# Performance work log

Hardware: AMD Instinct MI355X
Metric: run time of the kernel (lower is better)

The kernel has to match this reference:

```python
import jax, jax.numpy as jnp
import numpy as np


def _slice_coeffs(grid, guide):
    """Trilinear slice of bilateral grid at (x, y, guide) per full-res pixel.
    grid:  [B, C, D, Hg, Wg]  (C=12 affine coeffs)
    guide: [B, 1, H, W] in [0, 1]
    returns coeffs [B, C, H, W]
    """
    B, C, D, Hg, Wg = grid.shape
    H, W = guide.shape[2], guide.shape[3]
    g = guide[:, 0]  # [B, H, W]

    # HDRNet sampling convention: pixel centers mapped into grid coords
    gx = (jnp.arange(W, dtype=grid.dtype) + 0.5) / W * Wg - 0.5   # [W]
    gy = (jnp.arange(H, dtype=grid.dtype) + 0.5) / H * Hg - 0.5   # [H]
    gz = g * D - 0.5                                              # [B, H, W]

    gx = jnp.broadcast_to(gx[None, None, :], (B, H, W))
    gy = jnp.broadcast_to(gy[None, :, None], (B, H, W))

    fx0 = jnp.floor(gx); fy0 = jnp.floor(gy); fz0 = jnp.floor(gz)
    wx = gx - fx0; wy = gy - fy0; wz = gz - fz0  # trilinear fractions

    x0 = jnp.clip(fx0.astype(jnp.int32), 0, Wg - 1)
    x1 = jnp.clip(fx0.astype(jnp.int32) + 1, 0, Wg - 1)
    y0 = jnp.clip(fy0.astype(jnp.int32), 0, Hg - 1)
    y1 = jnp.clip(fy0.astype(jnp.int32) + 1, 0, Hg - 1)
    z0 = jnp.clip(fz0.astype(jnp.int32), 0, D - 1)
    z1 = jnp.clip(fz0.astype(jnp.int32) + 1, 0, D - 1)

    def gather_one(gb, zi, yi, xi):
        # gb: [C, D, Hg, Wg]; zi/yi/xi: [H, W] -> [C, H, W]
        return gb[:, zi, yi, xi]

    gather = jax.vmap(gather_one)  # over batch

    out = jnp.zeros((B, C, H, W), dtype=grid.dtype)
    for zi, wzc in ((z0, 1.0 - wz), (z1, wz)):
        for yi, wyc in ((y0, 1.0 - wy), (y1, wy)):
            for xi, wxc in ((x0, 1.0 - wx), (x1, wx)):
                w = (wzc * wyc * wxc)[:, None]  # [B, 1, H, W]
                out = out + w * gather(grid, zi, yi, xi)
    return out


def setup_inputs() -> dict:
    key = jax.random.key(0)
    k1, k2, k3 = jax.random.split(key, 3)
    Bilterial_Grid = jax.random.normal(k1, (4, 12, 8, 16, 16), dtype=jnp.float32)
    Guide = jax.random.uniform(k2, (4, 1, 1024, 1024), dtype=jnp.float32)
    fr = jax.random.uniform(k3, (4, 3, 1024, 1024), dtype=jnp.float32)
    return {"Bilterial_Grid": Bilterial_Grid, "Guide": Guide, "fr": fr}


def reference(Bilterial_Grid, Guide, fr):
    B, _, H, W = fr.shape
    coeffs = _slice_coeffs(Bilterial_Grid, Guide)          # [B, 12, H, W]
    co = coeffs.reshape(B, 3, 4, H, W)                      # 3x4 affine per pixel
    # out_c = sum_i A[c,i] * fr_i + b[c]
    out = jnp.einsum('boihw,bihw->bohw', co[:, :, :3], fr) + co[:, :, 3]
    return out
```

## Files before the change

### kernel.cpp

```cpp
#include <hip/hip_runtime.h>


#define ZSTRIDE 100

using half2v = decltype(__builtin_amdgcn_cvt_pkrtz(0.0f, 0.0f));

static __device__ __forceinline__ half2v pkrtz(float lo, float hi) {
    return __builtin_amdgcn_cvt_pkrtz(lo, hi);
}
static __device__ __forceinline__ half2v u2h2(unsigned int u) {
    return __builtin_bit_cast(half2v, u);
}
static __device__ __forceinline__ unsigned int h2u(half2v h) {
    return __builtin_bit_cast(unsigned int, h);
}

#if __has_builtin(__builtin_amdgcn_fdot2)
#define DOT2(d, wp, acc) __builtin_amdgcn_fdot2(u2h2(d), (wp), (acc), false)
#else
static __device__ __forceinline__ float dot2_sw(unsigned int d, half2v wp, float acc) {
    half2v h = u2h2(d);
    return fmaf((float)wp.x, (float)h.x, fmaf((float)wp.y, (float)h.y, acc));
}
#define DOT2(d, wp, acc) dot2_sw((d), (wp), (acc))
#endif

static __device__ __forceinline__ void corner_dot(
    const unsigned int* __restrict__ cp, half2v wp,
    float& a0, float& a1, float& a2, float& a3)
{
    const uint4 d = *reinterpret_cast<const uint4*>(cp);
    a0 = DOT2(d.x, wp, a0);
    a1 = DOT2(d.y, wp, a1);
    a2 = DOT2(d.z, wp, a2);
    a3 = DOT2(d.w, wp, a3);
}

__global__ __launch_bounds__(256, 8) void slice_apply(
    const float* __restrict__ grid,
    const float* __restrict__ guide,
    const float* __restrict__ fr,
    float* __restrict__ out)
{
    __shared__ __align__(16) unsigned int lds[8 * ZSTRIDE];

    const int b     = blockIdx.y;
    const int tileX = blockIdx.x & 15;
    const int tileY = blockIdx.x >> 4;
    const int t     = threadIdx.x;

    {
        const int yodd = tileY & 1;
        const int fy0  = (tileY >> 1) - 1 + yodd;
        const int ry0  = min(max(fy0, 0), 15);
        const int ry1  = min(max(fy0 + 1, 0), 15);
        const int px0  = min(max(tileX - 1, 0), 15);
        const int px1  = tileX;
        const int px2  = min(tileX + 1, 15);
        for (int e = t; e < 8 * 6 * 12; e += 256) {
            const int c    = e % 12;
            const int cell = (e / 12) % 6;
            const int s    = e / 72;
            const int s2   = min(s + 1, 7);
            const int yr   = cell / 3;
            const int xc   = cell % 3;
            const int ry = yr ? ry1 : ry0;
            const int rx = (xc == 0) ? px0 : ((xc == 1) ? px1 : px2);
            const int cb = (b * 12 + c) * 8;
            const int sp = ry * 16 + rx;
            const float lo = grid[(cb + s)  * 256 + sp];
            const float hi = grid[(cb + s2) * 256 + sp];
            lds[s * ZSTRIDE + cell * 12 + c] = h2u(pkrtz(lo, hi));
        }
    }
    __syncthreads();

    const int w   = t >> 6;
    const int l   = t & 63;
    const int by  = w >> 1;
    const int bx  = w & 1;
    const int lx  = l & 31;
    const int sub = l >> 5;

    const int tx  = bx * 32 + lx;
    const int xg  = tileX * 64 + tx;
    const int y0  = tileY * 32 + by * 16 + sub;
    int gofs = (b * 1024 + y0) * 1024 + xg;
    int fofs = ((b * 3) * 1024 + y0) * 1024 + xg;

    const float wx = ((float)tx + 0.5f) * 0.015625f + (0.5f - (float)bx);
    const float u1 = wx, u0 = 1.0f - wx;

    const int cof0 = (0 + bx) * 12;
    const int cof1 = (1 + bx) * 12;
    const int cof2 = (3 + bx) * 12;
    const int cof3 = (4 + bx) * 12;

    const float wyb = (tileY & 1) ? 0.0f : 0.5f;

    #pragma unroll 1
    for (int i = 0; i < 8; ++i) {
        const float g  = guide[gofs];
        const float f0 = fr[fofs];
        const float f1 = fr[fofs + 1048576];
        const float f2 = fr[fofs + 2097152];

        const int ly = by * 16 + i * 2 + sub;
        const float wy = ((float)ly + 0.5f) * 0.015625f + wyb;
        const float v1 = wy, v0 = 1.0f - wy;

        const float gz = g * 8.0f - 0.5f;
        int s = (int)floorf(gz);
        s = min(max(s, 0), 7);
        const float wz = fmaxf(gz - (float)s, 0.0f);
        const float zl = 1.0f - wz, zh = wz;
        const unsigned int* sb = &lds[s * ZSTRIDE];

        const float w00 = v0 * u0, w01 = v0 * u1;
        const float w10 = v1 * u0, w11 = v1 * u1;
        const half2v wp0 = pkrtz(w00 * zl, w00 * zh);
        const half2v wp1 = pkrtz(w01 * zl, w01 * zh);
        const half2v wp2 = pkrtz(w10 * zl, w10 * zh);
        const half2v wp3 = pkrtz(w11 * zl, w11 * zh);

        float o0, o1, o2;
        {
            float a0 = 0.f, a1 = 0.f, a2 = 0.f, a3 = 0.f;
            corner_dot(sb + cof0, wp0, a0, a1, a2, a3);
            corner_dot(sb + cof1, wp1, a0, a1, a2, a3);
            corner_dot(sb + cof2, wp2, a0, a1, a2, a3);
            corner_dot(sb + cof3, wp3, a0, a1, a2, a3);
            o0 = fmaf(a0, f0, fmaf(a1, f1, fmaf(a2, f2, a3)));
        }
        {
            float a0 = 0.f, a1 = 0.f, a2 = 0.f, a3 = 0.f;
            corner_dot(sb + cof0 + 4, wp0, a0, a1, a2, a3);
            corner_dot(sb + cof1 + 4, wp1, a0, a1, a2, a3);
            corner_dot(sb + cof2 + 4, wp2, a0, a1, a2, a3);
            corner_dot(sb + cof3 + 4, wp3, a0, a1, a2, a3);
            o1 = fmaf(a0, f0, fmaf(a1, f1, fmaf(a2, f2, a3)));
        }
        {
            float a0 = 0.f, a1 = 0.f, a2 = 0.f, a3 = 0.f;
            corner_dot(sb + cof0 + 8, wp0, a0, a1, a2, a3);
            corner_dot(sb + cof1 + 8, wp1, a0, a1, a2, a3);
            corner_dot(sb + cof2 + 8, wp2, a0, a1, a2, a3);
            corner_dot(sb + cof3 + 8, wp3, a0, a1, a2, a3);
            o2 = fmaf(a0, f0, fmaf(a1, f1, fmaf(a2, f2, a3)));
        }

        out[fofs]           = o0;
        out[fofs + 1048576] = o1;
        out[fofs + 2097152] = o2;

        gofs += 2 * 1024;
        fofs += 2 * 1024;
    }
}

extern "C" void kernel_launch(void* const* d_in, const int* in_sizes, int n_in,
                              void* d_out, int out_size, void* d_ws, size_t ws_size,
                              hipStream_t stream) {
    const float* grid  = (const float*)d_in[0];
    const float* guide = (const float*)d_in[1];
    const float* fr    = (const float*)d_in[2];
    float* out = (float*)d_out;

    dim3 g(512, 4);
    dim3 blk(256);
    hipLaunchKernelGGL(slice_apply, g, blk, 0, stream, grid, guide, fr, out);
}
```

Before: 119.4 us.

## Software-pipeline global and LDS loads across row iterations, fully unroll loop

Restructures the per-row loop into a software pipeline. Guide values are prefetched two rows ahead and fr values one row ahead. The LDS coefficient vectors for the next row are refilled right after each corner is consumed, and the loop is fully unrolled. The first global loads are issued before the grid-to-LDS staging so their latency overlaps it. The aim is to hide global memory and LDS latency behind the dot-product work, at the cost of many more live registers, so launch bounds drop from 8 to 4 waves-per-EU occupancy.

```diff
diff --git a/kernel.cpp b/kernel.cpp
--- a/kernel.cpp
+++ b/kernel.cpp
@@ -25,18 +25,20 @@
 #define DOT2(d, wp, acc) dot2_sw((d), (wp), (acc))
 #endif
 
-static __device__ __forceinline__ void corner_dot(
-    const unsigned int* __restrict__ cp, half2v wp,
-    float& a0, float& a1, float& a2, float& a3)
-{
-    const uint4 d = *reinterpret_cast<const uint4*>(cp);
-    a0 = DOT2(d.x, wp, a0);
-    a1 = DOT2(d.y, wp, a1);
-    a2 = DOT2(d.z, wp, a2);
-    a3 = DOT2(d.w, wp, a3);
-}
+#define CONSUME(qa, qb, qc, wp)                                   \
+    aA0 = DOT2((qa).x, (wp), aA0); aA1 = DOT2((qa).y, (wp), aA1); \
+    aA2 = DOT2((qa).z, (wp), aA2); aA3 = DOT2((qa).w, (wp), aA3); \
+    aB0 = DOT2((qb).x, (wp), aB0); aB1 = DOT2((qb).y, (wp), aB1); \
+    aB2 = DOT2((qb).z, (wp), aB2); aB3 = DOT2((qb).w, (wp), aB3); \
+    aC0 = DOT2((qc).x, (wp), aC0); aC1 = DOT2((qc).y, (wp), aC1); \
+    aC2 = DOT2((qc).z, (wp), aC2); aC3 = DOT2((qc).w, (wp), aC3);
 
-__global__ __launch_bounds__(256, 8) void slice_apply(
+#define REFILL(qa, qb, qc, cof)                                        \
+    qa = *reinterpret_cast<const uint4*>(sbn + (cof));                 \
+    qb = *reinterpret_cast<const uint4*>(sbn + (cof) + 4);             \
+    qc = *reinterpret_cast<const uint4*>(sbn + (cof) + 8);
+
+__global__ __launch_bounds__(256, 4) void slice_apply(
     const float* __restrict__ grid,
     const float* __restrict__ guide,
     const float* __restrict__ fr,
@@ -48,6 +50,25 @@
     const int tileX = blockIdx.x & 15;
     const int tileY = blockIdx.x >> 4;
     const int t     = threadIdx.x;
+
+    const int w   = t >> 6;
+    const int l   = t & 63;
+    const int by  = w >> 1;
+    const int bx  = w & 1;
+    const int lx  = l & 31;
+    const int sub = l >> 5;
+
+    const int tx  = bx * 32 + lx;
+    const int xg  = tileX * 64 + tx;
+    const int y0  = tileY * 32 + by * 16 + sub;
+    int gofs = (b * 1024 + y0) * 1024 + xg;
+    int fofs = ((b * 3) * 1024 + y0) * 1024 + xg;
+
+    float gcur = guide[gofs];
+    float gnx  = guide[gofs + 2048];
+    float f0c  = fr[fofs];
+    float f1c  = fr[fofs + 1048576];
+    float f2c  = fr[fofs + 2097152];
 
     {
         const int yodd = tileY & 1;
@@ -75,19 +96,6 @@
     }
     __syncthreads();
 
-    const int w   = t >> 6;
-    const int l   = t & 63;
-    const int by  = w >> 1;
-    const int bx  = w & 1;
-    const int lx  = l & 31;
-    const int sub = l >> 5;
-
-    const int tx  = bx * 32 + lx;
-    const int xg  = tileX * 64 + tx;
-    const int y0  = tileY * 32 + by * 16 + sub;
-    int gofs = (b * 1024 + y0) * 1024 + xg;
-    int fofs = ((b * 3) * 1024 + y0) * 1024 + xg;
-
     const float wx = ((float)tx + 0.5f) * 0.015625f + (0.5f - (float)bx);
     const float u1 = wx, u0 = 1.0f - wx;
 
@@ -98,24 +106,45 @@
 
     const float wyb = (tileY & 1) ? 0.0f : 0.5f;
 
-    #pragma unroll 1
+    uint4 q0a, q0b, q0c, q1a, q1b, q1c, q2a, q2b, q2c, q3a, q3b, q3c;
+    float wzc;
+    {
+        const float gz = gcur * 8.0f - 0.5f;
+        int s = (int)floorf(gz);
+        s = min(max(s, 0), 7);
+        wzc = fmaxf(gz - (float)s, 0.0f);
+        const unsigned int* sbn = &lds[s * ZSTRIDE];
+        REFILL(q0a, q0b, q0c, cof0)
+        REFILL(q1a, q1b, q1c, cof1)
+        REFILL(q2a, q2b, q2c, cof2)
+        REFILL(q3a, q3b, q3c, cof3)
+    }
+
+    float gn2 = 0.f, fn0 = 0.f, fn1 = 0.f, fn2 = 0.f;
+
+    #pragma unroll
     for (int i = 0; i < 8; ++i) {
-        const float g  = guide[gofs];
-        const float f0 = fr[fofs];
-        const float f1 = fr[fofs + 1048576];
-        const float f2 = fr[fofs + 2097152];
+        if (i < 6) gn2 = guide[gofs + 4096];
+        if (i < 7) {
+            fn0 = fr[fofs + 2048];
+            fn1 = fr[fofs + 2048 + 1048576];
+            fn2 = fr[fofs + 2048 + 2097152];
+        }
+
+        float wzn = 0.f;
+        const unsigned int* sbn = lds;
+        if (i < 7) {
+            const float gz = gnx * 8.0f - 0.5f;
+            int s = (int)floorf(gz);
+            s = min(max(s, 0), 7);
+            wzn = fmaxf(gz - (float)s, 0.0f);
+            sbn = &lds[s * ZSTRIDE];
+        }
 
         const int ly = by * 16 + i * 2 + sub;
         const float wy = ((float)ly + 0.5f) * 0.015625f + wyb;
         const float v1 = wy, v0 = 1.0f - wy;
-
-        const float gz = g * 8.0f - 0.5f;
-        int s = (int)floorf(gz);
-        s = min(max(s, 0), 7);
-        const float wz = fmaxf(gz - (float)s, 0.0f);
-        const float zl = 1.0f - wz, zh = wz;
-        const unsigned int* sb = &lds[s * ZSTRIDE];
-
+        const float zl = 1.0f - wzc, zh = wzc;
         const float w00 = v0 * u0, w01 = v0 * u1;
         const float w10 = v1 * u0, w11 = v1 * u1;
         const half2v wp0 = pkrtz(w00 * zl, w00 * zh);
@@ -123,38 +152,31 @@
         const half2v wp2 = pkrtz(w10 * zl, w10 * zh);
         const half2v wp3 = pkrtz(w11 * zl, w11 * zh);
 
-        float o0, o1, o2;
-        {
-            float a0 = 0.f, a1 = 0.f, a2 = 0.f, a3 = 0.f;
-            corner_dot(sb + cof0, wp0, a0, a1, a2, a3);
-            corner_dot(sb + cof1, wp1, a0, a1, a2, a3);
-            corner_dot(sb + cof2, wp2, a0, a1, a2, a3);
-            corner_dot(sb + cof3, wp3, a0, a1, a2, a3);
-            o0 = fmaf(a0, f0, fmaf(a1, f1, fmaf(a2, f2, a3)));
-        }
-        {
-            float a0 = 0.f, a1 = 0.f, a2 = 0.f, a3 = 0.f;
-            corner_dot(sb + cof0 + 4, wp0, a0, a1, a2, a3);
-            corner_dot(sb + cof1 + 4, wp1, a0, a1, a2, a3);
-            corner_dot(sb + cof2 + 4, wp2, a0, a1, a2, a3);
-            corner_dot(sb + cof3 + 4, wp3, a0, a1, a2, a3);
-            o1 = fmaf(a0, f0, fmaf(a1, f1, fmaf(a2, f2, a3)));
-        }
-        {
-            float a0 = 0.f, a1 = 0.f, a2 = 0.f, a3 = 0.f;
-            corner_dot(sb + cof0 + 8, wp0, a0, a1, a2, a3);
-            corner_dot(sb + cof1 + 8, wp1, a0, a1, a2, a3);
-            corner_dot(sb + cof2 + 8, wp2, a0, a1, a2, a3);
-            corner_dot(sb + cof3 + 8, wp3, a0, a1, a2, a3);
-            o2 = fmaf(a0, f0, fmaf(a1, f1, fmaf(a2, f2, a3)));
-        }
+        float aA0 = 0.f, aA1 = 0.f, aA2 = 0.f, aA3 = 0.f;
+        float aB0 = 0.f, aB1 = 0.f, aB2 = 0.f, aB3 = 0.f;
+        float aC0 = 0.f, aC1 = 0.f, aC2 = 0.f, aC3 = 0.f;
 
+        CONSUME(q0a, q0b, q0c, wp0)
+        if (i < 7) { REFILL(q0a, q0b, q0c, cof0) }
+        CONSUME(q1a, q1b, q1c, wp1)
+        if (i < 7) { REFILL(q1a, q1b, q1c, cof1) }
+        CONSUME(q2a, q2b, q2c, wp2)
+        if (i < 7) { REFILL(q2a, q2b, q2c, cof2) }
+        CONSUME(q3a, q3b, q3c, wp3)
+        if (i < 7) { REFILL(q3a, q3b, q3c, cof3) }
+
+        const float o0 = fmaf(aA0, f0c, fmaf(aA1, f1c, fmaf(aA2, f2c, aA3)));
+        const float o1 = fmaf(aB0, f0c, fmaf(aB1, f1c, fmaf(aB2, f2c, aB3)));
+        const float o2 = fmaf(aC0, f0c, fmaf(aC1, f1c, fmaf(aC2, f2c, aC3)));
         out[fofs]           = o0;
         out[fofs + 1048576] = o1;
         out[fofs + 2097152] = o2;
 
-        gofs += 2 * 1024;
-        fofs += 2 * 1024;
+        gnx = gn2;
+        f0c = fn0; f1c = fn1; f2c = fn2;
+        wzc = wzn;
+        gofs += 2048;
+        fofs += 2048;
     }
 }
 
```

New measurement: 120.9 us. No clear change (+1.3%).
